# Optimization experiments

Hardware: AMD Instinct MI355X
Metric: run time of the kernel (lower is better)

Reference implementation:

```python
import jax, jax.numpy as jnp
import numpy as np

B, C, H, W = 32, 1024, 32, 32  # NOTE: code requires C == H*W (see bmm below)
C_HALF = C // 2


def setup_inputs() -> dict:
    key = jax.random.key(0)
    ks = jax.random.split(key, 7)
    s_in = 1.0 / np.sqrt(C)
    return {
        "x": jax.random.normal(ks[0], (B, C, H, W), dtype=jnp.float32),
        "Wq": jax.random.normal(ks[1], (C_HALF, C), dtype=jnp.float32) * s_in,
        "bq": jax.random.normal(ks[2], (C_HALF,), dtype=jnp.float32) * 0.01,
        "Wk": jax.random.normal(ks[3], (C_HALF, C), dtype=jnp.float32) * s_in,
        "bk": jax.random.normal(ks[4], (C_HALF,), dtype=jnp.float32) * 0.01,
        "Wv": jax.random.normal(ks[5], (C, C), dtype=jnp.float32) * s_in,
        "bv": jax.random.normal(ks[6], (C,), dtype=jnp.float32) * 0.01,
    }


def reference(x, Wq, bq, Wk, bk, Wv, bv):
    b, c, h, w = x.shape
    hw = h * w
    xf = x.reshape(b, c, hw)  # [B, C, HW]
    # 1x1 convs are per-pixel linear maps over channels
    q = jnp.einsum('oc,bcn->bno', Wq, xf) + bq            # [B, HW, C/2]  (permuted)
    k = jnp.einsum('oc,bcn->bon', Wk, xf) + bk[:, None]   # [B, C/2, HW]
    v = jnp.einsum('oc,bcn->bno', Wv, xf) + bv            # [B, HW, C]   (permuted)
    attn = jax.nn.softmax(jnp.einsum('bno,bom->bnm', q, k), axis=-1)  # [B, HW, HW]
    # torch: bmm(value [B,HW,C], attention^T [B,HW,HW]) -> requires C == HW
    out = jnp.einsum('bik,bjk->bij', v, attn)  # [B, HW(=C), HW]
    out = out.reshape(b, c, h, w)
    return out + x
```

## Files before the change

kernel.cpp:

```cpp
#include <hip/hip_runtime.h>

typedef _Float16 f16;
typedef _Float16 f16x8 __attribute__((ext_vector_type(8)));
typedef float f32x4 __attribute__((ext_vector_type(4)));

__device__ __forceinline__ void g2lds16(const void* g, void* l) {
    __builtin_amdgcn_global_load_lds(
        (const __attribute__((address_space(1))) void*)g,
        (__attribute__((address_space(3))) void*)l, 16, 0, 0);
}

__global__ __launch_bounds__(256)
void prep_w(const float* __restrict__ Wq, const float* __restrict__ bq,
            const float* __restrict__ Wk, const float* __restrict__ bk,
            const float* __restrict__ Wv, const float* __restrict__ bv,
            f16* __restrict__ Wall, float* __restrict__ ball)
{
    const int idx = blockIdx.x * 256 + threadIdx.x;
    const int o = idx >> 10;
    const int c = idx & 1023;
    float w;
    if (o < 512)        w = Wq[idx];
    else if (o < 1024)  w = Wk[idx - 512 * 1024];
    else                w = Wv[idx - 1024 * 1024];
    Wall[idx] = (f16)w;
    if (c == 0)
        ball[o] = (o < 512) ? bq[o] : (o < 1024) ? bk[o - 512] : bv[o - 1024];
}

__global__ __launch_bounds__(256)
void transpose_cast(const float* __restrict__ x, f16* __restrict__ xT)
{
    __shared__ float t[32][33];
    const int b  = blockIdx.z;
    const int c0 = blockIdx.y << 5;
    const int n0 = blockIdx.x << 5;
    const int tx = threadIdx.x & 31, ty = threadIdx.x >> 5;
    const float* xb = x + (unsigned long long)b * (1024ull * 1024ull);
#pragma unroll
    for (int i = 0; i < 32; i += 8)
        t[ty + i][tx] = xb[(unsigned long long)(c0 + ty + i) * 1024ull + (n0 + tx)];
    __syncthreads();
    f16* ob = xT + (unsigned long long)b * (1024ull * 1024ull);
#pragma unroll
    for (int i = 0; i < 32; i += 8)
        ob[(unsigned long long)(n0 + ty + i) * 1024ull + (c0 + tx)] = (f16)t[tx][ty + i];
}

template <int EPI>
__global__ __launch_bounds__(256)
void gemm_nt(const f16* __restrict__ A, const f16* __restrict__ Bm,
             int lda, int ldb, int K,
             unsigned long long sA, unsigned long long sB,
             const float* __restrict__ bias,
             f16* __restrict__ Oh, float* __restrict__ Of,
             int ldo, unsigned long long sO,
             const float* __restrict__ Xres)
{
    __shared__ f16 As[128 * 32];
    __shared__ f16 Bs[128 * 32];

    const int tid  = threadIdx.x;
    const int wave = tid >> 6;
    const int lane = tid & 63;
    const int quad = lane >> 4;
    const int l16  = lane & 15;
    const int wr   = (wave >> 1) << 6;
    const int wc   = (wave & 1) << 6;

    const int bm = blockIdx.x << 7;
    const int bn = blockIdx.y << 7;
    const int bz = blockIdx.z;

    const f16* Ab = A  + (unsigned long long)bz * sA;
    const f16* Bb = Bm + (unsigned long long)bz * sB;

    const int srow = lane >> 2;
    const int scol = (lane & 3) << 3;

    f32x4 acc[4][4] = {};

    for (int k0 = 0; k0 < K; k0 += 32) {
        __syncthreads();
#pragma unroll
        for (int t = 0; t < 2; ++t) {
            const int rbase = t * 64 + wave * 16;
            g2lds16(Ab + (unsigned long long)(bm + rbase + srow) * (unsigned long long)lda + (k0 + scol),
                    As + rbase * 32 + lane * 8);
            g2lds16(Bb + (unsigned long long)(bn + rbase + srow) * (unsigned long long)ldb + (k0 + scol),
                    Bs + rbase * 32 + lane * 8);
        }
        __syncthreads();

        f16x8 af[4], bf[4];
#pragma unroll
        for (int i = 0; i < 4; ++i)
            af[i] = *(const f16x8*)(As + (wr + i * 16 + l16) * 32 + quad * 8);
#pragma unroll
        for (int i = 0; i < 4; ++i)
            bf[i] = *(const f16x8*)(Bs + (wc + i * 16 + l16) * 32 + quad * 8);

#pragma unroll
        for (int mi = 0; mi < 4; ++mi)
#pragma unroll
            for (int ni = 0; ni < 4; ++ni)
                acc[mi][ni] = __builtin_amdgcn_mfma_f32_16x16x32_f16(
                    af[mi], bf[ni], acc[mi][ni], 0, 0, 0);
    }

#pragma unroll
    for (int mi = 0; mi < 4; ++mi) {
#pragma unroll
        for (int v = 0; v < 4; ++v) {
            const int row = bm + wr + mi * 16 + quad * 4 + v;
#pragma unroll
            for (int ni = 0; ni < 4; ++ni) {
                const int col = bn + wc + ni * 16 + l16;
                float val = acc[mi][ni][v];
                if (EPI == 0) {
                    val += bias[col];
                    Oh[(unsigned long long)row * (unsigned long long)ldo + col] = (f16)val;
                } else if (EPI == 1) {
                    Of[(unsigned long long)bz * sO +
                       (unsigned long long)row * (unsigned long long)ldo + col] = val;
                } else {
                    const unsigned long long off =
                        (unsigned long long)bz * sO +
                        (unsigned long long)row * (unsigned long long)ldo + col;
                    Of[off] = val + Xres[off];
                }
            }
        }
    }
}

__global__ __launch_bounds__(256)
void softmax_rows(const float* __restrict__ S, f16* __restrict__ P)
{
    const unsigned long long row = blockIdx.x;
    const int tid = threadIdx.x;
    const float4 v = ((const float4*)(S + row * 1024ull))[tid];

    float m = fmaxf(fmaxf(v.x, v.y), fmaxf(v.z, v.w));
#pragma unroll
    for (int off = 32; off; off >>= 1)
        m = fmaxf(m, __shfl_xor(m, off, 64));

    __shared__ float redm[4], reds[4];
    const int wave = tid >> 6, lane = tid & 63;
    if (lane == 0) redm[wave] = m;
    __syncthreads();
    m = fmaxf(fmaxf(redm[0], redm[1]), fmaxf(redm[2], redm[3]));

    const float e0 = __expf(v.x - m), e1 = __expf(v.y - m);
    const float e2 = __expf(v.z - m), e3 = __expf(v.w - m);
    float sum = e0 + e1 + e2 + e3;
#pragma unroll
    for (int off = 32; off; off >>= 1)
        sum += __shfl_xor(sum, off, 64);
    if (lane == 0) reds[wave] = sum;
    __syncthreads();
    sum = reds[0] + reds[1] + reds[2] + reds[3];
    const float inv = 1.0f / sum;

    union { f16 h[4]; uint2 u; } pk;
    pk.h[0] = (f16)(e0 * inv); pk.h[1] = (f16)(e1 * inv);
    pk.h[2] = (f16)(e2 * inv); pk.h[3] = (f16)(e3 * inv);
    ((uint2*)(P + row * 1024ull))[tid] = pk.u;
}

extern "C" void kernel_launch(void* const* d_in, const int* in_sizes, int n_in,
                              void* d_out, int out_size, void* d_ws, size_t ws_size,
                              hipStream_t stream)
{
    const float* x  = (const float*)d_in[0];
    const float* Wq = (const float*)d_in[1];
    const float* bq = (const float*)d_in[2];
    const float* Wk = (const float*)d_in[3];
    const float* bk = (const float*)d_in[4];
    const float* Wv = (const float*)d_in[5];
    const float* bv = (const float*)d_in[6];
    float* out = (float*)d_out;

    f16*   xT   = (f16*)d_ws;
    f16*   Wall = xT + 32ull * 1024 * 1024;
    float* ball = (float*)(Wall + 2048ull * 1024);
    f16*   QKV  = (f16*)(ball + 2048);
    float* S    = (float*)(QKV + 64ull * 1024 * 1024);
    f16*   P    = (f16*)(S + 32ull * 1024 * 1024);

    prep_w<<<8192, 256, 0, stream>>>(Wq, bq, Wk, bk, Wv, bv, Wall, ball);
    transpose_cast<<<dim3(32, 32, 32), 256, 0, stream>>>(x, xT);

    gemm_nt<0><<<dim3(256, 16, 1), 256, 0, stream>>>(
        xT, Wall, 1024, 1024, 1024, 0ull, 0ull,
        ball, QKV, nullptr, 2048, 0ull, nullptr);

    gemm_nt<1><<<dim3(8, 8, 32), 256, 0, stream>>>(
        QKV, QKV + 512, 2048, 2048, 512,
        1024ull * 2048ull, 1024ull * 2048ull,
        nullptr, nullptr, S, 1024, 1024ull * 1024ull, nullptr);

    softmax_rows<<<32768, 256, 0, stream>>>(S, P);

    gemm_nt<2><<<dim3(8, 8, 32), 256, 0, stream>>>(
        QKV + 1024, P, 2048, 1024, 1024,
        1024ull * 2048ull, 1024ull * 1024ull,
        nullptr, nullptr, out, 1024, 1024ull * 1024ull, x);
}
```

Before: 714.5 us.

## Deepen GEMM K-step to 64, template strides, swizzle QKV projection tiles

Each main-loop iteration of the GEMM now stages two 32-wide K slices into LDS, giving a 64-wide K step. This halves the number of barrier pairs per tile and doubles the MFMA work between barriers. Leading dimensions, K and batch strides become template constants so the compiler can fold the address arithmetic and unroll loops with fixed trip counts. The QKV projection launch becomes a 1D grid with a grouped swizzle (groups of 8 M-tiles across all N-tiles) to improve L2 reuse of the A rows. The cost is doubled LDS use per block, which may lower occupancy.

```diff
diff --git a/kernel.cpp b/kernel.cpp
--- a/kernel.cpp
+++ b/kernel.cpp
@@ -47,18 +47,16 @@
         ob[(unsigned long long)(n0 + ty + i) * 1024ull + (c0 + tx)] = (f16)t[tx][ty + i];
 }
 
-template <int EPI>
+template <int EPI, int LDA, int LDB, int K, int LDO,
+          long long SA, long long SB, long long SO, int SWZ>
 __global__ __launch_bounds__(256)
 void gemm_nt(const f16* __restrict__ A, const f16* __restrict__ Bm,
-             int lda, int ldb, int K,
-             unsigned long long sA, unsigned long long sB,
              const float* __restrict__ bias,
              f16* __restrict__ Oh, float* __restrict__ Of,
-             int ldo, unsigned long long sO,
              const float* __restrict__ Xres)
 {
-    __shared__ f16 As[128 * 32];
-    __shared__ f16 Bs[128 * 32];
+    __shared__ f16 As[2 * 128 * 32];
+    __shared__ f16 Bs[2 * 128 * 32];
 
     const int tid  = threadIdx.x;
     const int wave = tid >> 6;
@@ -68,44 +66,58 @@
     const int wr   = (wave >> 1) << 6;
     const int wc   = (wave & 1) << 6;
 
-    const int bm = blockIdx.x << 7;
-    const int bn = blockIdx.y << 7;
+    int bm, bn;
+    if (SWZ) {
+        const int g = blockIdx.x >> 7;
+        const int r = blockIdx.x & 127;
+        bm = ((g << 3) | (r & 7)) << 7;
+        bn = (r >> 3) << 7;
+    } else {
+        bm = blockIdx.x << 7;
+        bn = blockIdx.y << 7;
+    }
     const int bz = blockIdx.z;
 
-    const f16* Ab = A  + (unsigned long long)bz * sA;
-    const f16* Bb = Bm + (unsigned long long)bz * sB;
+    const f16* Ab = A  + (unsigned long long)bz * (unsigned long long)SA;
+    const f16* Bb = Bm + (unsigned long long)bz * (unsigned long long)SB;
 
     const int srow = lane >> 2;
     const int scol = (lane & 3) << 3;
 
     f32x4 acc[4][4] = {};
 
-    for (int k0 = 0; k0 < K; k0 += 32) {
+    for (int k0 = 0; k0 < K; k0 += 64) {
         __syncthreads();
 #pragma unroll
-        for (int t = 0; t < 2; ++t) {
-            const int rbase = t * 64 + wave * 16;
-            g2lds16(Ab + (unsigned long long)(bm + rbase + srow) * (unsigned long long)lda + (k0 + scol),
-                    As + rbase * 32 + lane * 8);
-            g2lds16(Bb + (unsigned long long)(bn + rbase + srow) * (unsigned long long)ldb + (k0 + scol),
-                    Bs + rbase * 32 + lane * 8);
+        for (int kk = 0; kk < 2; ++kk) {
+#pragma unroll
+            for (int t = 0; t < 2; ++t) {
+                const int rbase = t * 64 + wave * 16;
+                g2lds16(Ab + (unsigned long long)(bm + rbase + srow) * LDA + (k0 + kk * 32 + scol),
+                        As + kk * 4096 + rbase * 32 + lane * 8);
+                g2lds16(Bb + (unsigned long long)(bn + rbase + srow) * LDB + (k0 + kk * 32 + scol),
+                        Bs + kk * 4096 + rbase * 32 + lane * 8);
+            }
         }
         __syncthreads();
 
-        f16x8 af[4], bf[4];
-#pragma unroll
-        for (int i = 0; i < 4; ++i)
-            af[i] = *(const f16x8*)(As + (wr + i * 16 + l16) * 32 + quad * 8);
-#pragma unroll
-        for (int i = 0; i < 4; ++i)
-            bf[i] = *(const f16x8*)(Bs + (wc + i * 16 + l16) * 32 + quad * 8);
-
-#pragma unroll
-        for (int mi = 0; mi < 4; ++mi)
-#pragma unroll
-            for (int ni = 0; ni < 4; ++ni)
-                acc[mi][ni] = __builtin_amdgcn_mfma_f32_16x16x32_f16(
-                    af[mi], bf[ni], acc[mi][ni], 0, 0, 0);
+#pragma unroll
+        for (int kk = 0; kk < 2; ++kk) {
+            f16x8 af[4], bf[4];
+#pragma unroll
+            for (int i = 0; i < 4; ++i)
+                af[i] = *(const f16x8*)(As + kk * 4096 + (wr + i * 16 + l16) * 32 + quad * 8);
+#pragma unroll
+            for (int i = 0; i < 4; ++i)
+                bf[i] = *(const f16x8*)(Bs + kk * 4096 + (wc + i * 16 + l16) * 32 + quad * 8);
+
+#pragma unroll
+            for (int mi = 0; mi < 4; ++mi)
+#pragma unroll
+                for (int ni = 0; ni < 4; ++ni)
+                    acc[mi][ni] = __builtin_amdgcn_mfma_f32_16x16x32_f16(
+                        af[mi], bf[ni], acc[mi][ni], 0, 0, 0);
+        }
     }
 
 #pragma unroll
@@ -119,14 +131,14 @@
                 float val = acc[mi][ni][v];
                 if (EPI == 0) {
                     val += bias[col];
-                    Oh[(unsigned long long)row * (unsigned long long)ldo + col] = (f16)val;
+                    Oh[(unsigned long long)row * LDO + col] = (f16)val;
                 } else if (EPI == 1) {
-                    Of[(unsigned long long)bz * sO +
-                       (unsigned long long)row * (unsigned long long)ldo + col] = val;
+                    Of[(unsigned long long)bz * (unsigned long long)SO +
+                       (unsigned long long)row * LDO + col] = val;
                 } else {
                     const unsigned long long off =
-                        (unsigned long long)bz * sO +
-                        (unsigned long long)row * (unsigned long long)ldo + col;
+                        (unsigned long long)bz * (unsigned long long)SO +
+                        (unsigned long long)row * LDO + col;
                     Of[off] = val + Xres[off];
                 }
             }
@@ -192,19 +204,17 @@
     prep_w<<<8192, 256, 0, stream>>>(Wq, bq, Wk, bk, Wv, bv, Wall, ball);
     transpose_cast<<<dim3(32, 32, 32), 256, 0, stream>>>(x, xT);
 
-    gemm_nt<0><<<dim3(256, 16, 1), 256, 0, stream>>>(
-        xT, Wall, 1024, 1024, 1024, 0ull, 0ull,
-        ball, QKV, nullptr, 2048, 0ull, nullptr);
-
-    gemm_nt<1><<<dim3(8, 8, 32), 256, 0, stream>>>(
-        QKV, QKV + 512, 2048, 2048, 512,
-        1024ull * 2048ull, 1024ull * 2048ull,
-        nullptr, nullptr, S, 1024, 1024ull * 1024ull, nullptr);
+    gemm_nt<0, 1024, 1024, 1024, 2048, 0ll, 0ll, 0ll, 1>
+        <<<dim3(4096, 1, 1), 256, 0, stream>>>(
+        xT, Wall, ball, QKV, nullptr, nullptr);
+
+    gemm_nt<1, 2048, 2048, 512, 1024, 1024ll * 2048, 1024ll * 2048, 1024ll * 1024, 0>
+        <<<dim3(8, 8, 32), 256, 0, stream>>>(
+        QKV, QKV + 512, nullptr, nullptr, S, nullptr);
 
     softmax_rows<<<32768, 256, 0, stream>>>(S, P);
 
-    gemm_nt<2><<<dim3(8, 8, 32), 256, 0, stream>>>(
-        QKV + 1024, P, 2048, 1024, 1024,
-        1024ull * 2048ull, 1024ull * 1024ull,
-        nullptr, nullptr, out, 1024, 1024ull * 1024ull, x);
-}
+    gemm_nt<2, 2048, 1024, 1024, 1024, 1024ll * 2048, 1024ll * 1024, 1024ll * 1024, 0>
+        <<<dim3(8, 8, 32), 256, 0, stream>>>(
+        QKV + 1024, P, nullptr, nullptr, out, x);
+}
```

Result: faster. 644.4 us (-9.8%).
